# Performance work log

Hardware: AMD Instinct MI355X
Metric: run time of the kernel (lower is better)

## Reference

```python
import jax, jax.numpy as jnp
import numpy as np
from jax import lax

NUM_HEADS = 16
DIM = 1024
BATCH = 4
SEQ = 2048


def setup_inputs() -> dict:
    key = jax.random.key(0)
    ks = jax.random.split(key, 12)
    f32 = jnp.float32
    q = jax.random.normal(ks[0], (BATCH, SEQ, DIM), dtype=f32)
    k = jax.random.normal(ks[1], (BATCH, SEQ, DIM), dtype=f32)
    v = jax.random.normal(ks[2], (BATCH, SEQ, DIM), dtype=f32)
    lim = 1.0 / np.sqrt(DIM)  # nn.Linear default init range
    Wi = jax.random.uniform(ks[3], (DIM, DIM), minval=-lim, maxval=lim, dtype=f32)
    bi = jax.random.uniform(ks[4], (DIM,), minval=-lim, maxval=lim, dtype=f32)
    Wg = jax.random.uniform(ks[5], (DIM, DIM), minval=-lim, maxval=lim, dtype=f32)
    bg = jax.random.uniform(ks[6], (DIM,), minval=-lim, maxval=lim, dtype=f32)
    Wo = jax.random.uniform(ks[7], (DIM, DIM), minval=-lim, maxval=lim, dtype=f32)
    bo = jax.random.uniform(ks[8], (DIM,), minval=-lim, maxval=lim, dtype=f32)
    A = jax.random.normal(ks[9], (DIM, DIM), dtype=f32) * 0.1
    Bm = jax.random.normal(ks[10], (DIM, DIM), dtype=f32) * 0.1
    decay = jnp.full((1, NUM_HEADS, 1), 0.9, dtype=f32)
    return dict(q=q, k=k, v=v, Wi=Wi, bi=bi, Wg=Wg, bg=bg, A=A, Bm=Bm,
                Wo=Wo, bo=bo, decay=decay)


def reference(q, k, v, Wi, bi, Wg, bg, A, Bm, Wo, bo, decay):
    B, S, D = q.shape
    H = decay.shape[1]
    hd = D // H
    # time-major heads: [S, B, H, hd]
    qh = jnp.moveaxis(q.reshape(B, S, H, hd), 1, 0)
    kh = jnp.moveaxis(k.reshape(B, S, H, hd), 1, 0)
    vh = jnp.moveaxis(v.reshape(B, S, H, hd), 1, 0)

    def step(carry, xs):
        r, state = carry
        qt, kt, vt = xs
        r = decay * r + kt * vt                         # [B, H, hd]
        retained = (qt * r).reshape(B, D)               # [B, D]
        inp = retained @ Wi.T + bi
        gate = jax.nn.sigmoid(inp @ Wg.T + bg)
        blended = gate * state + (1.0 - gate) * inp
        state = jnp.tanh(blended @ A.T + inp @ Bm.T)
        out = state @ Wo.T + bo                         # [B, D]
        return (r, state), out

    r0 = jnp.zeros((B, H, hd), dtype=q.dtype)
    s0 = jnp.zeros((B, D), dtype=q.dtype)
    _, outs = lax.scan(step, (r0, s0), (qh, kh, vh))     # outs: [S, B, D]
    return jnp.moveaxis(outs, 0, 1)                      # [B, S, D]
```

## Files before the change

### kernel.cpp

```cpp
#include <hip/hip_runtime.h>
#include <hip/hip_bf16.h>
#include <math.h>

#define BATCH 4
#define SEQ   2048
#define DIM   1024
#define MROWS (SEQ*BATCH)
#define BIGN  ((size_t)MROWS*DIM)

typedef float v2f __attribute__((ext_vector_type(2)));

__global__ __launch_bounds__(256) void scan_a(const float* __restrict__ K,
    const float* __restrict__ V, const float* __restrict__ dec_p,
    float* __restrict__ E)
{
  int id  = blockIdx.x*256 + threadIdx.x;
  int c   = id >> 12;
  int rem = id & 4095;
  int b   = rem >> 10;
  int dc  = rem & 1023;
  float dec = dec_p[dc >> 6];
  size_t base = ((size_t)b*SEQ + (size_t)c*32)*DIM + dc;
  float r = 0.f;
  #pragma unroll 4
  for (int i = 0; i < 32; ++i) {
    float kv = K[base + (size_t)i*DIM] * V[base + (size_t)i*DIM];
    r = fmaf(dec, r, kv);
  }
  E[(size_t)c*4096 + rem] = r;
}

__global__ __launch_bounds__(256) void scan_b(const float* __restrict__ E,
    const float* __restrict__ dec_p, float* __restrict__ carry)
{
  int id = blockIdx.x*256 + threadIdx.x;
  int dc = id & 1023;
  float dec = dec_p[dc >> 6];
  float d2 = dec*dec, d4 = d2*d2, d8 = d4*d4, d16 = d8*d8, d32 = d16*d16;
  float r = 0.f;
  #pragma unroll 1
  for (int c = 0; c < 64; ++c) {
    carry[(size_t)c*4096 + id] = r;
    r = fmaf(d32, r, E[(size_t)c*4096 + id]);
  }
}

__global__ __launch_bounds__(256) void scan_c(const float* __restrict__ Q,
    const float* __restrict__ K, const float* __restrict__ V,
    const float* __restrict__ dec_p, const float* __restrict__ carry,
    float* __restrict__ ret)
{
  int id  = blockIdx.x*256 + threadIdx.x;
  int c   = id >> 12;
  int rem = id & 4095;
  int b   = rem >> 10;
  int dc  = rem & 1023;
  float dec = dec_p[dc >> 6];
  size_t base = ((size_t)b*SEQ + (size_t)c*32)*DIM + dc;
  float r = carry[(size_t)c*4096 + rem];
  #pragma unroll 1
  for (int i = 0; i < 32; ++i) {
    int t = c*32 + i;
    float kv = K[base + (size_t)i*DIM] * V[base + (size_t)i*DIM];
    r = fmaf(dec, r, kv);
    ret[((size_t)t*BATCH + b)*DIM + dc] = Q[base + (size_t)i*DIM] * r;
  }
}

#define GM 64
#define GN 64
#define GK 32
#define LDA 68

template<int MODE>
__global__ __launch_bounds__(256) void gemm_k(
    const float* __restrict__ X, const float* __restrict__ W,
    const float* __restrict__ bias, float* __restrict__ C,
    const float* __restrict__ inp, float* __restrict__ u_out,
    float* __restrict__ outf)
{
  __shared__ float Xs[GK][LDA];
  __shared__ float Ws[GK][LDA];
  const int tid = threadIdx.x;
  const int m0 = blockIdx.y * GM;
  const int n0 = blockIdx.x * GN;
  const int tx = tid & 15, ty = tid >> 4;
  v2f acc[4][2] = {};
  #pragma unroll 1
  for (int kb = 0; kb < DIM; kb += GK) {
    #pragma unroll
    for (int h = 0; h < 2; ++h) {
      int idx = tid + h*256;
      int row = idx >> 3;
      int kc  = (idx & 7) << 2;
      float4 xv = *(const float4*)(X + (size_t)(m0+row)*DIM + kb + kc);
      Xs[kc+0][row] = xv.x; Xs[kc+1][row] = xv.y;
      Xs[kc+2][row] = xv.z; Xs[kc+3][row] = xv.w;
      float4 wv = *(const float4*)(W + (size_t)(n0+row)*DIM + kb + kc);
      Ws[kc+0][row] = wv.x; Ws[kc+1][row] = wv.y;
      Ws[kc+2][row] = wv.z; Ws[kc+3][row] = wv.w;
    }
    __syncthreads();
    #pragma unroll
    for (int kk = 0; kk < GK; ++kk) {
      float4 a = *(const float4*)&Xs[kk][ty << 2];
      float4 w = *(const float4*)&Ws[kk][tx << 2];
      v2f w0 = {w.x, w.y};
      v2f w1 = {w.z, w.w};
      float av[4] = {a.x, a.y, a.z, a.w};
      #pragma unroll
      for (int i = 0; i < 4; ++i) {
        v2f ab = {av[i], av[i]};
        acc[i][0] = __builtin_elementwise_fma(ab, w0, acc[i][0]);
        acc[i][1] = __builtin_elementwise_fma(ab, w1, acc[i][1]);
      }
    }
    __syncthreads();
  }
  float bj[4];
  #pragma unroll
  for (int j = 0; j < 4; ++j)
    bj[j] = (MODE == 0 || MODE == 1 || MODE == 3) ? bias[n0 + (tx<<2) + j] : 0.f;
  #pragma unroll
  for (int i = 0; i < 4; ++i) {
    int m = m0 + (ty<<2) + i;
    #pragma unroll
    for (int j = 0; j < 4; ++j) {
      int n = n0 + (tx<<2) + j;
      size_t off = (size_t)m*DIM + n;
      float vv = acc[i][j >> 1][j & 1] + bj[j];
      if (MODE == 2) vv += C[off];
      if (MODE == 1) {
        float gv = 1.f/(1.f + expf(-vv));
        C[off] = gv;
        u_out[off] = (1.f - gv) * inp[off];
      } else if (MODE == 3) {
        outf[((size_t)(m & 3)*SEQ + (size_t)(m >> 2))*DIM + n] = vv;
      } else {
        C[off] = vv;
      }
    }
  }
}

#define RBLK 64

__global__ __launch_bounds__(512, 2) void recur_k(
    const float* __restrict__ A, const float* __restrict__ g,
    const float* __restrict__ dpre, float* __restrict__ s,
    unsigned long long* __restrict__ sf)
{
  __shared__ __align__(16) float xs[8*132 + 4];
  const int tid = threadIdx.x;
  const int w   = tid >> 6;
  const int ln  = tid & 63;
  const int b   = blockIdx.x >> 4;
  const int blk = blockIdx.x & 15;
  const int row = blk*64 + w*8 + (ln >> 3);
  const int ks  = ln & 7;

  const size_t slotstride = (size_t)BATCH*DIM;
  unsigned long long* sfb = sf + (size_t)b*DIM;

  float4 areg[32];
  #pragma unroll
  for (int j = 0; j < 32; ++j)
    areg[j] = *(const float4*)(A + (size_t)row*DIM + ks*128 + 4*j);
  const v2f* a2 = reinterpret_cast<const v2f*>(areg);

  const int xoff = (tid >> 6)*132 + ((2*tid) & 127);

  #pragma unroll 1
  for (int t = 0; t < SEQ; ++t) {
    float2 gv = *(const float2*)(g + ((size_t)t*4 + b)*DIM + 2*tid);
    float dval = (ks == 0) ? dpre[((size_t)t*4 + b)*DIM + row] : 0.f;

    v2f acc0 = {0.f, 0.f}, acc1 = {0.f, 0.f};
    v2f acc2 = {0.f, 0.f}, acc3 = {0.f, 0.f};
    if (t > 0) {
      unsigned long long* p0 = sfb + (size_t)((t-1)&1)*slotstride + 2*tid;
      const unsigned want = (unsigned)t;
      union { unsigned long long u; unsigned ui[2]; float f[2]; } a0, a1;
      int guard = 0;
      for (;;) {
        a0.u = __hip_atomic_load(p0,     __ATOMIC_RELAXED,
                                 __HIP_MEMORY_SCOPE_AGENT);
        a1.u = __hip_atomic_load(p0 + 1, __ATOMIC_RELAXED,
                                 __HIP_MEMORY_SCOPE_AGENT);
        if ((a0.ui[1] == want && a1.ui[1] == want) || ++guard > (1 << 25))
          break;
      }

      *(float2*)(xs + xoff) = make_float2(gv.x * a0.f[0], gv.y * a1.f[0]);
      asm volatile("s_waitcnt lgkmcnt(0)\n\ts_barrier" ::: "memory");

      const float* xb = xs + ks*132;
      #pragma unroll
      for (int j = 0; j < 32; j += 4) {
        float4 x0 = *(const float4*)(xb + 4*j);
        float4 x1 = *(const float4*)(xb + 4*j + 4);
        float4 x2 = *(const float4*)(xb + 4*j + 8);
        float4 x3 = *(const float4*)(xb + 4*j + 12);
        v2f x0l = {x0.x, x0.y}, x0h = {x0.z, x0.w};
        v2f x1l = {x1.x, x1.y}, x1h = {x1.z, x1.w};
        v2f x2l = {x2.x, x2.y}, x2h = {x2.z, x2.w};
        v2f x3l = {x3.x, x3.y}, x3h = {x3.z, x3.w};
        acc0 = __builtin_elementwise_fma(a2[2*j+0], x0l, acc0);
        acc0 = __builtin_elementwise_fma(a2[2*j+1], x0h, acc0);
        acc1 = __builtin_elementwise_fma(a2[2*j+2], x1l, acc1);
        acc1 = __builtin_elementwise_fma(a2[2*j+3], x1h, acc1);
        acc2 = __builtin_elementwise_fma(a2[2*j+4], x2l, acc2);
        acc2 = __builtin_elementwise_fma(a2[2*j+5], x2h, acc2);
        acc3 = __builtin_elementwise_fma(a2[2*j+6], x3l, acc3);
        acc3 = __builtin_elementwise_fma(a2[2*j+7], x3h, acc3);
      }
    }
    v2f accp = (acc0 + acc1) + (acc2 + acc3);
    float sum = accp.x + accp.y;
    sum += __shfl_xor(sum, 1, 64);
    sum += __shfl_xor(sum, 2, 64);
    sum += __shfl_xor(sum, 4, 64);
    if (ks == 0) {
      float val = tanhf(sum + dval);
      union { unsigned long long u; unsigned ui[2]; float f[2]; } pk;
      pk.f[0] = val; pk.ui[1] = (unsigned)(t + 1);
      __hip_atomic_store(sfb + (size_t)(t & 1)*slotstride + row, pk.u,
                         __ATOMIC_RELAXED, __HIP_MEMORY_SCOPE_AGENT);
      s[((size_t)t*4 + b)*DIM + row] = val;
    }
    asm volatile("s_barrier" ::: "memory");
  }
}

extern "C" void kernel_launch(void* const* d_in, const int* in_sizes, int n_in,
                              void* d_out, int out_size, void* d_ws, size_t ws_size,
                              hipStream_t stream)
{
  (void)in_sizes; (void)n_in; (void)out_size;
  const float* q   = (const float*)d_in[0];
  const float* k   = (const float*)d_in[1];
  const float* v   = (const float*)d_in[2];
  const float* Wi  = (const float*)d_in[3];
  const float* bi  = (const float*)d_in[4];
  const float* Wg  = (const float*)d_in[5];
  const float* bg  = (const float*)d_in[6];
  const float* A   = (const float*)d_in[7];
  const float* Bm  = (const float*)d_in[8];
  const float* Wo  = (const float*)d_in[9];
  const float* bo  = (const float*)d_in[10];
  const float* dec = (const float*)d_in[11];

  const size_t sf_bytes = (size_t)2*BATCH*DIM*sizeof(unsigned long long);
  size_t need = (4*BIGN + 2*(size_t)64*4096)*sizeof(float) + sf_bytes;
  if (ws_size < need) return;

  float* b0 = (float*)d_ws;
  float* b1 = b0 + BIGN;
  float* b2 = b1 + BIGN;
  float* b3 = b2 + BIGN;
  float* E     = b3 + BIGN;
  float* carry = E + (size_t)64*4096;
  unsigned long long* sf = (unsigned long long*)(carry + (size_t)64*4096);
  float* outp  = (float*)d_out;

  hipMemsetAsync(sf, 0, sf_bytes, stream);

  scan_a<<<1024, 256, 0, stream>>>(k, v, dec, E);
  scan_b<<<16,   256, 0, stream>>>(E, dec, carry);
  scan_c<<<1024, 256, 0, stream>>>(q, k, v, dec, carry, b0);

  dim3 gg(DIM/GN, MROWS/GM);
  gemm_k<0><<<gg, 256, 0, stream>>>(b0, Wi, bi, b1, nullptr, nullptr, nullptr);
  gemm_k<1><<<gg, 256, 0, stream>>>(b1, Wg, bg, b2, b1, b0, nullptr);
  gemm_k<4><<<gg, 256, 0, stream>>>(b0, A,  nullptr, b3, nullptr, nullptr, nullptr);
  gemm_k<2><<<gg, 256, 0, stream>>>(b1, Bm, nullptr, b3, nullptr, nullptr, nullptr);

  recur_k<<<RBLK, 512, 0, stream>>>(A, b2, b3, b0, sf);

  gemm_k<3><<<gg, 256, 0, stream>>>(b0, Wo, bo, nullptr, nullptr, nullptr, outp);
}
```

Baseline: 5.078 ms.

## Pack state flags into float LSBs, double-buffer recurrence smem, enlarge GEMM tiles

The recurrence kernel now packs two state values per 64-bit word and uses a parity bit in each float's LSB as the readiness tag, replacing the separate timestep tag. This halves the flag traffic and the spin loads. It also prefetches the next step's gate and input values and speculatively samples the flags before the next iteration. It double-buffers the shared x vector so the trailing barrier can be dropped, and swaps tanhf for an exp2/rcp approximation. Separately, the GEMM tile grows from 64x64 to 128x128 with an 8x8 per-thread block. The risks are slightly lossy state precision from the overwritten LSB and tanh approximation error.

```diff
diff --git a/kernel.cpp b/kernel.cpp
--- a/kernel.cpp
+++ b/kernel.cpp
@@ -67,10 +67,10 @@
   }
 }
 
-#define GM 64
-#define GN 64
-#define GK 32
-#define LDA 68
+#define GM 128
+#define GN 128
+#define GK 16
+#define LDG 132
 
 template<int MODE>
 __global__ __launch_bounds__(256) void gemm_k(
@@ -79,54 +79,58 @@
     const float* __restrict__ inp, float* __restrict__ u_out,
     float* __restrict__ outf)
 {
-  __shared__ float Xs[GK][LDA];
-  __shared__ float Ws[GK][LDA];
+  __shared__ float Xs[GK][LDG];
+  __shared__ float Ws[GK][LDG];
   const int tid = threadIdx.x;
   const int m0 = blockIdx.y * GM;
   const int n0 = blockIdx.x * GN;
   const int tx = tid & 15, ty = tid >> 4;
-  v2f acc[4][2] = {};
+  v2f acc[8][4] = {};
   #pragma unroll 1
   for (int kb = 0; kb < DIM; kb += GK) {
     #pragma unroll
     for (int h = 0; h < 2; ++h) {
       int idx = tid + h*256;
-      int row = idx >> 3;
-      int kc  = (idx & 7) << 2;
-      float4 xv = *(const float4*)(X + (size_t)(m0+row)*DIM + kb + kc);
-      Xs[kc+0][row] = xv.x; Xs[kc+1][row] = xv.y;
-      Xs[kc+2][row] = xv.z; Xs[kc+3][row] = xv.w;
-      float4 wv = *(const float4*)(W + (size_t)(n0+row)*DIM + kb + kc);
-      Ws[kc+0][row] = wv.x; Ws[kc+1][row] = wv.y;
-      Ws[kc+2][row] = wv.z; Ws[kc+3][row] = wv.w;
+      int r   = idx >> 2;
+      int kc  = (idx & 3) << 2;
+      float4 xv = *(const float4*)(X + (size_t)(m0+r)*DIM + kb + kc);
+      Xs[kc+0][r] = xv.x; Xs[kc+1][r] = xv.y;
+      Xs[kc+2][r] = xv.z; Xs[kc+3][r] = xv.w;
+      float4 wv2 = *(const float4*)(W + (size_t)(n0+r)*DIM + kb + kc);
+      Ws[kc+0][r] = wv2.x; Ws[kc+1][r] = wv2.y;
+      Ws[kc+2][r] = wv2.z; Ws[kc+3][r] = wv2.w;
     }
     __syncthreads();
     #pragma unroll
     for (int kk = 0; kk < GK; ++kk) {
-      float4 a = *(const float4*)&Xs[kk][ty << 2];
-      float4 w = *(const float4*)&Ws[kk][tx << 2];
-      v2f w0 = {w.x, w.y};
-      v2f w1 = {w.z, w.w};
-      float av[4] = {a.x, a.y, a.z, a.w};
+      float4 a0 = *(const float4*)&Xs[kk][ty*8];
+      float4 a1 = *(const float4*)&Xs[kk][ty*8 + 4];
+      float4 w0 = *(const float4*)&Ws[kk][tx*4];
+      float4 w1 = *(const float4*)&Ws[kk][64 + tx*4];
+      v2f wv[4] = {{w0.x,w0.y},{w0.z,w0.w},{w1.x,w1.y},{w1.z,w1.w}};
+      float av[8] = {a0.x,a0.y,a0.z,a0.w,a1.x,a1.y,a1.z,a1.w};
       #pragma unroll
-      for (int i = 0; i < 4; ++i) {
+      for (int i = 0; i < 8; ++i) {
         v2f ab = {av[i], av[i]};
-        acc[i][0] = __builtin_elementwise_fma(ab, w0, acc[i][0]);
-        acc[i][1] = __builtin_elementwise_fma(ab, w1, acc[i][1]);
+        #pragma unroll
+        for (int j = 0; j < 4; ++j)
+          acc[i][j] = __builtin_elementwise_fma(ab, wv[j], acc[i][j]);
       }
     }
     __syncthreads();
   }
-  float bj[4];
+  float bj[8];
   #pragma unroll
-  for (int j = 0; j < 4; ++j)
-    bj[j] = (MODE == 0 || MODE == 1 || MODE == 3) ? bias[n0 + (tx<<2) + j] : 0.f;
+  for (int j = 0; j < 8; ++j) {
+    int n = n0 + ((j < 4) ? (tx*4 + j) : (64 + tx*4 + (j - 4)));
+    bj[j] = (MODE == 0 || MODE == 1 || MODE == 3) ? bias[n] : 0.f;
+  }
   #pragma unroll
-  for (int i = 0; i < 4; ++i) {
-    int m = m0 + (ty<<2) + i;
+  for (int i = 0; i < 8; ++i) {
+    int m = m0 + ty*8 + i;
     #pragma unroll
-    for (int j = 0; j < 4; ++j) {
-      int n = n0 + (tx<<2) + j;
+    for (int j = 0; j < 8; ++j) {
+      int n = n0 + ((j < 4) ? (tx*4 + j) : (64 + tx*4 + (j - 4)));
       size_t off = (size_t)m*DIM + n;
       float vv = acc[i][j >> 1][j & 1] + bj[j];
       if (MODE == 2) vv += C[off];
@@ -150,7 +154,7 @@
     const float* __restrict__ dpre, float* __restrict__ s,
     unsigned long long* __restrict__ sf)
 {
-  __shared__ __align__(16) float xs[8*132 + 4];
+  __shared__ __align__(16) float xs[2][8*132 + 4];
   const int tid = threadIdx.x;
   const int w   = tid >> 6;
   const int ln  = tid & 63;
@@ -159,8 +163,8 @@
   const int row = blk*64 + w*8 + (ln >> 3);
   const int ks  = ln & 7;
 
-  const size_t slotstride = (size_t)BATCH*DIM;
-  unsigned long long* sfb = sf + (size_t)b*DIM;
+  const size_t slotstride = (size_t)BATCH*512;
+  unsigned long long* sfb = sf + (size_t)b*512;
 
   float4 areg[32];
   #pragma unroll
@@ -170,31 +174,39 @@
 
   const int xoff = (tid >> 6)*132 + ((2*tid) & 127);
 
+  float2 gvc = *(const float2*)(g + (size_t)b*DIM + 2*tid);
+  float  dvc = (ks == 0) ? dpre[(size_t)b*DIM + row] : 0.f;
+  unsigned long long sampA = 0, sampB = 0;
+
   #pragma unroll 1
   for (int t = 0; t < SEQ; ++t) {
-    float2 gv = *(const float2*)(g + ((size_t)t*4 + b)*DIM + 2*tid);
-    float dval = (ks == 0) ? dpre[((size_t)t*4 + b)*DIM + row] : 0.f;
-
-    v2f acc0 = {0.f, 0.f}, acc1 = {0.f, 0.f};
-    v2f acc2 = {0.f, 0.f}, acc3 = {0.f, 0.f};
+    const int buf = t & 1;
+    v2f acc0 = {0.f,0.f}, acc1 = {0.f,0.f}, acc2 = {0.f,0.f}, acc3 = {0.f,0.f};
     if (t > 0) {
-      unsigned long long* p0 = sfb + (size_t)((t-1)&1)*slotstride + 2*tid;
-      const unsigned want = (unsigned)t;
-      union { unsigned long long u; unsigned ui[2]; float f[2]; } a0, a1;
-      int guard = 0;
-      for (;;) {
-        a0.u = __hip_atomic_load(p0,     __ATOMIC_RELAXED,
-                                 __HIP_MEMORY_SCOPE_AGENT);
-        a1.u = __hip_atomic_load(p0 + 1, __ATOMIC_RELAXED,
-                                 __HIP_MEMORY_SCOPE_AGENT);
-        if ((a0.ui[1] == want && a1.ui[1] == want) || ++guard > (1 << 25))
-          break;
+      const unsigned wl = ((unsigned)(t + 1) >> 1) & 1u;
+      unsigned long long* pw =
+          sfb + (size_t)((t - 1) & 1)*slotstride + tid;
+      union { unsigned long long u; float f[2]; } wv;
+      if ((unsigned)(sampA & 1u) == wl)       wv.u = sampA;
+      else if ((unsigned)(sampB & 1u) == wl)  wv.u = sampB;
+      else {
+        int guard = 0;
+        for (;;) {
+          unsigned long long x0 = __hip_atomic_load(pw, __ATOMIC_RELAXED,
+                                                    __HIP_MEMORY_SCOPE_AGENT);
+          unsigned long long x1 = __hip_atomic_load(pw, __ATOMIC_RELAXED,
+                                                    __HIP_MEMORY_SCOPE_AGENT);
+          if ((unsigned)(x0 & 1u) == wl) { wv.u = x0; break; }
+          if ((unsigned)(x1 & 1u) == wl) { wv.u = x1; break; }
+          if (++guard > (1 << 22))       { wv.u = x1; break; }
+        }
       }
 
-      *(float2*)(xs + xoff) = make_float2(gv.x * a0.f[0], gv.y * a1.f[0]);
+      *(float2*)(xs[buf] + xoff) = make_float2(gvc.x * wv.f[0],
+                                               gvc.y * wv.f[1]);
       asm volatile("s_waitcnt lgkmcnt(0)\n\ts_barrier" ::: "memory");
 
-      const float* xb = xs + ks*132;
+      const float* xb = xs[buf] + ks*132;
       #pragma unroll
       for (int j = 0; j < 32; j += 4) {
         float4 x0 = *(const float4*)(xb + 4*j);
@@ -220,15 +232,34 @@
     sum += __shfl_xor(sum, 1, 64);
     sum += __shfl_xor(sum, 2, 64);
     sum += __shfl_xor(sum, 4, 64);
+    float val = 0.f;
     if (ks == 0) {
-      float val = tanhf(sum + dval);
-      union { unsigned long long u; unsigned ui[2]; float f[2]; } pk;
-      pk.f[0] = val; pk.ui[1] = (unsigned)(t + 1);
-      __hip_atomic_store(sfb + (size_t)(t & 1)*slotstride + row, pk.u,
+      float zz  = sum + dvc;
+      float e2x = __builtin_amdgcn_exp2f(zz * 2.8853900817779268f);
+      val = 1.0f - 2.0f * __builtin_amdgcn_rcpf(e2x + 1.0f);
+    }
+    float pv = __shfl_xor(val, 8, 64);
+    const unsigned tg = ((unsigned)(t + 2) >> 1) & 1u;
+    if ((ln & 15) == 0) {
+      union { unsigned long long u; unsigned ui[2]; } pk;
+      pk.ui[0] = (__float_as_uint(val) & ~1u) | tg;
+      pk.ui[1] = (__float_as_uint(pv)  & ~1u) | tg;
+      __hip_atomic_store(sfb + (size_t)(t & 1)*slotstride + (row >> 1), pk.u,
                          __ATOMIC_RELAXED, __HIP_MEMORY_SCOPE_AGENT);
+    }
+    if (ks == 0)
       s[((size_t)t*4 + b)*DIM + row] = val;
-    }
-    asm volatile("s_barrier" ::: "memory");
+
+    if (t + 1 < SEQ) {
+      gvc = *(const float2*)(g + ((size_t)(t + 1)*4 + b)*DIM + 2*tid);
+      dvc = (ks == 0) ? dpre[((size_t)(t + 1)*4 + b)*DIM + row] : 0.f;
+      unsigned long long* pw1 = sfb + (size_t)(t & 1)*slotstride + tid;
+      sampA = __hip_atomic_load(pw1, __ATOMIC_RELAXED,
+                                __HIP_MEMORY_SCOPE_AGENT);
+      sampB = __hip_atomic_load(pw1, __ATOMIC_RELAXED,
+                                __HIP_MEMORY_SCOPE_AGENT);
+      asm volatile("" ::: "memory");
+    }
   }
 }
 
@@ -250,7 +281,7 @@
   const float* bo  = (const float*)d_in[10];
   const float* dec = (const float*)d_in[11];
 
-  const size_t sf_bytes = (size_t)2*BATCH*DIM*sizeof(unsigned long long);
+  const size_t sf_bytes = (size_t)2*BATCH*512*sizeof(unsigned long long);
   size_t need = (4*BIGN + 2*(size_t)64*4096)*sizeof(float) + sf_bytes;
   if (ws_size < need) return;
 
```

After: 5.892 ms. 1.16x slower.
